# Kernel optimization log

Hardware: AMD Instinct MI355X
Metric: run time of the kernel (lower is better)

Reference implementation:

```python
import jax, jax.numpy as jnp
import numpy as np

N = 50000      # nodes
E = 800000     # edges (avg degree 16)
DIN = 500      # input_dim
HID = 100      # hid_dim (fixed in module)
DOUT = 64      # output_dim
EPS = 1e-5     # LayerNorm eps (torch default)


def _layer_norm(x, g, b):
    mu = jnp.mean(x, axis=-1, keepdims=True)
    var = jnp.var(x, axis=-1, keepdims=True)
    return (x - mu) / jnp.sqrt(var + EPS) * g + b


def _gcn_conv(x, src, tgt, W, b):
    # PyG GCNConv: self-loops + symmetric normalization + linear + scatter-add
    h = x @ W  # [N, out]
    idx = jnp.arange(N)
    src_sl = jnp.concatenate([src, idx])
    tgt_sl = jnp.concatenate([tgt, idx])
    deg = jax.ops.segment_sum(jnp.ones(src_sl.shape, h.dtype), tgt_sl, num_segments=N)
    dinv = jnp.where(deg > 0, deg ** -0.5, 0.0)
    norm = dinv[src_sl] * dinv[tgt_sl]  # [E+N]
    out = jax.ops.segment_sum(h[src_sl] * norm[:, None], tgt_sl, num_segments=N)
    return out + b


def setup_inputs() -> dict:
    key = jax.random.key(0)
    ks = jax.random.split(key, 10)
    glorot = lambda k, fi, fo: jax.random.normal(k, (fi, fo), jnp.float32) * np.float32(1.0 / np.sqrt(fi))
    z = lambda d: jnp.zeros((d,), jnp.float32)
    return dict(
        data_x=jax.random.normal(ks[0], (N, DIN), jnp.float32),
        data_edge_index=jax.random.randint(ks[1], (2, E), 0, N),
        data_edge_attr=jnp.zeros((E,), jnp.int32),  # single relation type
        t_W1=glorot(ks[2], DIN, HID), t_b1=z(HID), t_g1=jnp.ones((HID,), jnp.float32), t_be1=z(HID),
        t_W2=glorot(ks[3], HID, HID), t_b2=z(HID), t_g2=jnp.ones((HID,), jnp.float32), t_be2=z(HID),
        r_Wrel=glorot(ks[4], HID, HID)[None],  # [n_relations=1, H, H]
        r_Wself=glorot(ks[5], HID, HID), r_b=z(HID),
        c1_W=glorot(ks[6], HID, HID), c1_b=z(HID),
        c2_W=glorot(ks[7], HID, DOUT), c2_b=z(DOUT),
    )


def reference(data_x, data_edge_index, data_edge_attr,
              t_W1, t_b1, t_g1, t_be1, t_W2, t_b2, t_g2, t_be2,
              r_Wrel, r_Wself, r_b, c1_W, c1_b, c2_W, c2_b):
    src, tgt = data_edge_index[0], data_edge_index[1]
    # transform: Linear -> LN -> ReLU -> Linear -> LN -> ReLU
    x = jax.nn.relu(_layer_norm(data_x @ t_W1 + t_b1, t_g1, t_be1))
    x = jax.nn.relu(_layer_norm(x @ t_W2 + t_b2, t_g2, t_be2))
    # RGCN, n_relations=1, n_layers=1: per-relation message + self transform
    msgs = x[src] @ r_Wrel[0]  # edge_attr is all relation 0
    x = x @ r_Wself + jax.ops.segment_sum(msgs, tgt, num_segments=N) + r_b
    x = jax.nn.relu(x)  # dropout = identity (eval)
    x = jax.nn.relu(_gcn_conv(x, src, tgt, c1_W, c1_b))
    x = _gcn_conv(x, src, tgt, c2_W, c2_b)
    return jax.nn.log_softmax(x, axis=1)
```

## Files before the change

kernel.cpp:

```cpp
#include <hip/hip_runtime.h>
#include <hip/hip_bf16.h>

typedef __attribute__((ext_vector_type(8))) short short8;
typedef __attribute__((ext_vector_type(8))) unsigned short ushort8;
typedef __attribute__((ext_vector_type(4))) float f32x4;

static constexpr int NN = 50000;
static constexpr int NE = 800000;
static constexpr int SCAN_B = 196;
static constexpr int NBLK = (NN + 63) / 64;

#define MFMA16x16x32 __builtin_amdgcn_mfma_f32_16x16x32_bf16

__device__ __forceinline__ float b2f(unsigned short u){
  unsigned v = ((unsigned)u) << 16;
  return __builtin_bit_cast(float, v);
}
__device__ __forceinline__ unsigned short f2b(float f){
  unsigned x = __builtin_bit_cast(unsigned, f);
  unsigned r = (x + 0x7fffu + ((x >> 16) & 1u)) >> 16;
  return (unsigned short)r;
}
__device__ __forceinline__ short8 u2s(ushort8 v){
  return __builtin_bit_cast(short8, v);
}

__device__ __align__(256) int   g_isf32;
__device__ __align__(256) unsigned short g_W1t  [112 * 512];
__device__ __align__(256) unsigned short g_W2t  [112 * 128];
__device__ __align__(256) unsigned short g_WselfT[112 * 128];
__device__ __align__(256) unsigned short g_WrelT [112 * 128];
__device__ __align__(256) unsigned short g_c1Wt [112 * 128];
__device__ __align__(256) unsigned short g_c2Wt [64 * 128];
__device__ __align__(256) unsigned short g_bufA[(size_t)NN * 128];
__device__ __align__(256) unsigned short g_bufB[(size_t)NN * 128];
__device__ __align__(256) unsigned short g_bufC[(size_t)NN * 128];
__device__ __align__(256) int   g_deg[NN];
__device__ __align__(256) int   g_rowptr[NN + 1];
__device__ __align__(256) int   g_cursor[NN];
__device__ __align__(256) int   g_colidx[NE];
__device__ __align__(256) float g_dinv[NN];
__device__ __align__(256) int   g_partial[256];

__device__ __forceinline__ float ld_in(const void* p, int idx, int isf32){
  if (isf32) return ((const float*)p)[idx];
  return b2f(((const unsigned short*)p)[idx]);
}

__global__ void k_detect_zero(const unsigned short* __restrict__ x){
  if (blockIdx.x == 0){
    __shared__ int sh[256];
    int tid = threadIdx.x;
    int cnt = 0;
    for (int j = 0; j < 16; j++){
      unsigned short h = x[(size_t)(tid * 16 + j) * 2];
      int e = (h >> 7) & 0xFF;
      if (e >= 90 && e <= 160) cnt++;
    }
    sh[tid] = cnt;
    __syncthreads();
    for (int off = 128; off > 0; off >>= 1){
      if (tid < off) sh[tid] += sh[tid + off];
      __syncthreads();
    }
    if (tid == 0) g_isf32 = (sh[0] < 2458) ? 1 : 0;
  } else {
    int i = (blockIdx.x - 1) * 256 + threadIdx.x;
    if (i < NN){ g_deg[i] = 0; g_cursor[i] = 0; }
  }
}

__device__ __forceinline__ void xp_one(const void* W, unsigned short* Wt, int idx,
                                       int K, int Nc, int Kpad, int Npad, int isf32){
  int n = idx / Kpad;
  int k = idx - n * Kpad;
  float v = 0.f;
  if (n < Nc && k < K) v = ld_in(W, k * Nc + n, isf32);
  Wt[(k >> 5) * (Npad * 32) + n * 32 + (k & 31)] = f2b(v);
}
__global__ void k_transpose_all(const void* W1, const void* W2, const void* Wself,
                                const void* Wrel, const void* c1W, const void* c2W){
  int idx = blockIdx.x * 256 + threadIdx.x;
  const int isf32 = g_isf32;
  if (idx < 57344){ xp_one(W1, g_W1t, idx, 500, 100, 512, 112, isf32); return; }
  idx -= 57344;
  if (idx < 14336){ xp_one(W2,    g_W2t,    idx, 100, 100, 128, 112, isf32); return; }
  idx -= 14336;
  if (idx < 14336){ xp_one(Wself, g_WselfT, idx, 100, 100, 128, 112, isf32); return; }
  idx -= 14336;
  if (idx < 14336){ xp_one(Wrel,  g_WrelT,  idx, 100, 100, 128, 112, isf32); return; }
  idx -= 14336;
  if (idx < 14336){ xp_one(c1W,   g_c1Wt,   idx, 100, 100, 128, 112, isf32); return; }
  idx -= 14336;
  if (idx < 8192){  xp_one(c2W,   g_c2Wt,   idx, 100, 64,  128, 64, isf32); }
}

__global__ void k_deg(const int* __restrict__ tgt){
  int e = blockIdx.x * 256 + threadIdx.x;
  if (e < NE) atomicAdd(&g_deg[tgt[e]], 1);
}
__global__ __launch_bounds__(256) void k_scan1(){
  __shared__ int sh[256];
  int t = threadIdx.x;
  int i = blockIdx.x * 256 + t;
  int val = (i < NN) ? g_deg[i] : 0;
  sh[t] = val; __syncthreads();
#pragma unroll
  for (int off = 1; off < 256; off <<= 1){
    int v = (t >= off) ? sh[t - off] : 0;
    __syncthreads(); sh[t] += v; __syncthreads();
  }
  if (i < NN){ g_rowptr[i] = sh[t] - val; g_dinv[i] = rsqrtf((float)(val + 1)); }
  if (t == 255) g_partial[blockIdx.x] = sh[255];
}
__global__ __launch_bounds__(256) void k_scan2(){
  __shared__ int sh[256];
  int t = threadIdx.x;
  int val = (t < SCAN_B) ? g_partial[t] : 0;
  sh[t] = val; __syncthreads();
#pragma unroll
  for (int off = 1; off < 256; off <<= 1){
    int v = (t >= off) ? sh[t - off] : 0;
    __syncthreads(); sh[t] += v; __syncthreads();
  }
  if (t < SCAN_B) g_partial[t] = sh[t] - val;
  if (t == 255) g_rowptr[NN] = sh[255];
}
__global__ __launch_bounds__(256) void k_scan3(){
  int i = blockIdx.x * 256 + threadIdx.x;
  if (i < NN) g_rowptr[i] += g_partial[blockIdx.x];
}
__global__ void k_fill(const int* __restrict__ src, const int* __restrict__ tgt){
  int e = blockIdx.x * 256 + threadIdx.x;
  if (e >= NE) return;
  int t = tgt[e];
  int pos = g_rowptr[t] + atomicAdd(&g_cursor[t], 1);
  g_colidx[pos] = src[e];
}


template<int DO_LN>
__device__ __forceinline__ void wave_epi(const f32x4* acc, unsigned short* dst,
    int rstride, int grow0, int lane, int isf32,
    const void* bias, const void* gm, const void* be){
  const int m = lane & 15;
  const int q = lane >> 4;
  float bf_[7], gf_[7], ef_[7];
#pragma unroll
  for (int t = 0; t < 7; t++){
    int col = t * 16 + m;
    bool ok = col < 100;
    bf_[t] = ok ? ld_in(bias, col, isf32) : 0.f;
    if (DO_LN){
      gf_[t] = ok ? ld_in(gm, col, isf32) : 0.f;
      ef_[t] = ok ? ld_in(be, col, isf32) : 0.f;
    }
  }
#pragma unroll
  for (int r = 0; r < 4; r++){
    int rl = q * 4 + r;
    float vals[7], s1 = 0.f, s2 = 0.f;
#pragma unroll
    for (int t = 0; t < 7; t++){
      int col = t * 16 + m;
      float v = (col < 100) ? (acc[t][r] + bf_[t]) : 0.f;
      vals[t] = v; s1 += v; s2 += v * v;
    }
    if (DO_LN){
#pragma unroll
      for (int msk = 1; msk < 16; msk <<= 1){
        s1 += __shfl_xor(s1, msk, 64);
        s2 += __shfl_xor(s2, msk, 64);
      }
      float mu = s1 * 0.01f;
      float var = fmaxf(s2 * 0.01f - mu * mu, 0.f);
      float rstd = rsqrtf(var + 1e-5f);
#pragma unroll
      for (int t = 0; t < 7; t++)
        vals[t] = (vals[t] - mu) * rstd * gf_[t] + ef_[t];
    }
    if (grow0 + rl < NN){
      unsigned short* orow = dst + (size_t)rl * rstride;
#pragma unroll
      for (int t = 0; t < 7; t++){
        int col = t * 16 + m;
        float y = fmaxf(vals[t], 0.f);
        orow[col] = f2b((col < 100) ? y : 0.f);
      }
      orow[112 + m] = 0;
    }
  }
}

template<int MODE>
__device__ __forceinline__ void agg_tile(const unsigned short* __restrict__ x,
    unsigned short* aggT, int tid, int brow0){
  const int nl = tid >> 2;
  const int c0 = (tid & 3) * 32;
  const int node = min(brow0 + nl, NN - 1);
  const float wt = (MODE != 0) ? g_dinv[node] : 1.f;
  float a[32];
#pragma unroll
  for (int k = 0; k < 32; k++) a[k] = 0.f;
  const int p0 = g_rowptr[node], p1 = g_rowptr[node + 1];
  for (int p = p0; p < p1; p += 4){
    int s[4]; float wj[4];
#pragma unroll
    for (int j = 0; j < 4; j++){
      bool ok = (p + j) < p1;
      s[j] = ok ? g_colidx[p + j] : node;
      wj[j] = ok ? ((MODE != 0) ? g_dinv[s[j]] * wt : 1.f) : 0.f;
    }
    ushort8 r[4][4];
#pragma unroll
    for (int j = 0; j < 4; j++)
#pragma unroll
      for (int u = 0; u < 4; u++)
        r[j][u] = *reinterpret_cast<const ushort8*>(&x[(size_t)s[j] * 128 + c0 + u * 8]);
#pragma unroll
    for (int j = 0; j < 4; j++)
#pragma unroll
      for (int u = 0; u < 4; u++)
#pragma unroll
        for (int k = 0; k < 8; k++)
          a[u * 8 + k] += wj[j] * b2f((unsigned short)r[j][u][k]);
  }
  if (MODE != 0){
    float ws = wt * wt;
#pragma unroll
    for (int u = 0; u < 4; u++){
      ushort8 sv = *reinterpret_cast<const ushort8*>(&x[(size_t)node * 128 + c0 + u * 8]);
#pragma unroll
      for (int k = 0; k < 8; k++) a[u * 8 + k] += ws * b2f((unsigned short)sv[k]);
    }
  }
  unsigned short* arow = aggT + nl * 136 + c0;
#pragma unroll
  for (int u = 0; u < 4; u++){
    ushort8 o;
#pragma unroll
    for (int k = 0; k < 8; k++) o[k] = f2b(a[u * 8 + k]);
    *reinterpret_cast<ushort8*>(&arow[u * 8]) = o;
  }
}


__global__ __launch_bounds__(256, 3) void k_gemm12(const void* __restrict__ Aext,
    const void* b1, const void* gm1, const void* be1,
    const void* b2, const void* gm2, const void* be2){
  __shared__ unsigned short xT[4][16][136];
  const int tid = threadIdx.x;
  const int w = tid >> 6, lane = tid & 63;
  const int m = lane & 15, q = lane >> 4;
  const int row0 = blockIdx.x * 64 + w * 16;
  const int isf32 = g_isf32;
  const int arow = min(row0 + m, NN - 1);

  f32x4 acc[7] = {};
  if (isf32){
    const float* base = (const float*)Aext + (size_t)arow * 500;
#pragma unroll
    for (int h = 0; h < 2; h++){
      f32x4 Ab[16];
#pragma unroll
      for (int kc = 0; kc < 8; kc++){
        int col = (h * 8 + kc) * 32 + q * 8;
        Ab[2 * kc]     = *reinterpret_cast<const f32x4*>(base + min(col, 496));
        Ab[2 * kc + 1] = *reinterpret_cast<const f32x4*>(base + min(col + 4, 496));
      }
      __builtin_amdgcn_sched_barrier(0);
#pragma unroll
      for (int kc = 0; kc < 8; kc++){
        f32x4 lo = Ab[2 * kc], hi = Ab[2 * kc + 1];
        short8 a = {(short)f2b(lo[0]), (short)f2b(lo[1]), (short)f2b(lo[2]), (short)f2b(lo[3]),
                    (short)f2b(hi[0]), (short)f2b(hi[1]), (short)f2b(hi[2]), (short)f2b(hi[3])};
        const unsigned short* bp = g_W1t + (h * 8 + kc) * 3584 + m * 32 + q * 8;
#pragma unroll
        for (int t = 0; t < 7; t++){
          short8 b = *reinterpret_cast<const short8*>(bp + t * 512);
          acc[t] = MFMA16x16x32(a, b, acc[t], 0, 0, 0);
        }
      }
    }
  } else {
    const unsigned short* base = (const unsigned short*)Aext + (size_t)arow * 500;
    ushort4 Ab[32];
#pragma unroll
    for (int kc = 0; kc < 16; kc++){
      int col = kc * 32 + q * 8;
      Ab[2 * kc]     = *reinterpret_cast<const ushort4*>(base + min(col, 496));
      Ab[2 * kc + 1] = *reinterpret_cast<const ushort4*>(base + min(col + 4, 496));
    }
    __builtin_amdgcn_sched_barrier(0);
#pragma unroll
    for (int kc = 0; kc < 16; kc++){
      ushort4 lo = Ab[2 * kc], hi = Ab[2 * kc + 1];
      short8 a = {(short)lo.x, (short)lo.y, (short)lo.z, (short)lo.w,
                  (short)hi.x, (short)hi.y, (short)hi.z, (short)hi.w};
      const unsigned short* bp = g_W1t + kc * 3584 + m * 32 + q * 8;
#pragma unroll
      for (int t = 0; t < 7; t++){
        short8 b = *reinterpret_cast<const short8*>(bp + t * 512);
        acc[t] = MFMA16x16x32(a, b, acc[t], 0, 0, 0);
      }
    }
  }
  wave_epi<1>(acc, &xT[w][0][0], 136, 0, lane, isf32, b1, gm1, be1);

  f32x4 acc2[7] = {};
#pragma unroll
  for (int kc = 0; kc < 4; kc++){
    int k0 = kc * 32 + q * 8;
    short8 a = u2s(*reinterpret_cast<const ushort8*>(&xT[w][m][k0]));
    const unsigned short* bp = g_W2t + kc * 3584 + m * 32 + q * 8;
#pragma unroll
    for (int t = 0; t < 7; t++){
      short8 b = *reinterpret_cast<const short8*>(bp + t * 512);
      acc2[t] = MFMA16x16x32(a, b, acc2[t], 0, 0, 0);
    }
  }
  wave_epi<1>(acc2, g_bufB + (size_t)row0 * 128, 128, row0, lane, isf32, b2, gm2, be2);
}

__global__ __launch_bounds__(256, 3) void k_rgcn_f(const void* rb){
  __shared__ unsigned short aggT[64 * 136];
  const int tid = threadIdx.x;
  const int brow0 = blockIdx.x * 64;
  agg_tile<0>(g_bufB, aggT, tid, brow0);

  const int w = tid >> 6, lane = tid & 63;
  const int m = lane & 15, q = lane >> 4;
  const int row0 = brow0 + w * 16;
  const int arow = min(row0 + m, NN - 1);
  const int isf32 = g_isf32;
  f32x4 acc[7] = {};
#pragma unroll
  for (int kc = 0; kc < 4; kc++){
    int k0 = kc * 32 + q * 8;
    short8 a1 = u2s(*reinterpret_cast<const ushort8*>(&g_bufB[(size_t)arow * 128 + k0]));
    const unsigned short* bp1 = g_WselfT + kc * 3584 + m * 32 + q * 8;
#pragma unroll
    for (int t = 0; t < 7; t++){
      short8 b = *reinterpret_cast<const short8*>(bp1 + t * 512);
      acc[t] = MFMA16x16x32(a1, b, acc[t], 0, 0, 0);
    }
    short8 a2 = u2s(*reinterpret_cast<const ushort8*>(&aggT[(w * 16 + m) * 136 + k0]));
    const unsigned short* bp2 = g_WrelT + kc * 3584 + m * 32 + q * 8;
#pragma unroll
    for (int t = 0; t < 7; t++){
      short8 b = *reinterpret_cast<const short8*>(bp2 + t * 512);
      acc[t] = MFMA16x16x32(a2, b, acc[t], 0, 0, 0);
    }
  }
  wave_epi<0>(acc, g_bufC + (size_t)row0 * 128, 128, row0, lane, isf32, rb, nullptr, nullptr);
}

__global__ __launch_bounds__(256, 3) void k_conv_f(const void* c1b){
  __shared__ unsigned short aggT[64 * 136];
  const int tid = threadIdx.x;
  const int brow0 = blockIdx.x * 64;
  agg_tile<1>(g_bufC, aggT, tid, brow0);

  const int w = tid >> 6, lane = tid & 63;
  const int m = lane & 15, q = lane >> 4;
  const int row0 = brow0 + w * 16;
  const int isf32 = g_isf32;
  unsigned short* tile = aggT + w * 16 * 136;

  f32x4 acc[7] = {};
#pragma unroll
  for (int kc = 0; kc < 4; kc++){
    int k0 = kc * 32 + q * 8;
    short8 a = u2s(*reinterpret_cast<const ushort8*>(&tile[m * 136 + k0]));
    const unsigned short* bp = g_c1Wt + kc * 3584 + m * 32 + q * 8;
#pragma unroll
    for (int t = 0; t < 7; t++){
      short8 b = *reinterpret_cast<const short8*>(bp + t * 512);
      acc[t] = MFMA16x16x32(a, b, acc[t], 0, 0, 0);
    }
  }
  wave_epi<0>(acc, tile, 136, 0, lane, isf32, c1b, nullptr, nullptr);

  f32x4 acc2[4] = {};
#pragma unroll
  for (int kc = 0; kc < 4; kc++){
    int k0 = kc * 32 + q * 8;
    short8 a = u2s(*reinterpret_cast<const ushort8*>(&tile[m * 136 + k0]));
    const unsigned short* bp = g_c2Wt + kc * 2048 + m * 32 + q * 8;
#pragma unroll
    for (int t = 0; t < 4; t++){
      short8 b = *reinterpret_cast<const short8*>(bp + t * 512);
      acc2[t] = MFMA16x16x32(a, b, acc2[t], 0, 0, 0);
    }
  }
#pragma unroll
  for (int r = 0; r < 4; r++){
    int row = row0 + q * 4 + r;
    if (row < NN){
      unsigned short* orow = g_bufA + (size_t)row * 64;
#pragma unroll
      for (int t = 0; t < 4; t++) orow[t * 16 + m] = f2b(acc2[t][r]);
    }
  }
}

__global__ __launch_bounds__(256) void k_agg_lsm(const void* __restrict__ bias,
                                                 void* __restrict__ outv){
  const int isf32 = g_isf32;
  int node = blockIdx.x * 32 + (threadIdx.x >> 3);
  if (node >= NN) return;
  const int c8 = (threadIdx.x & 7) * 8;
  float wt = g_dinv[node];
  float a[4][8];
#pragma unroll
  for (int j = 0; j < 4; j++)
#pragma unroll
    for (int k = 0; k < 8; k++) a[j][k] = 0.f;
  int p0 = g_rowptr[node], p1 = g_rowptr[node + 1];
  for (int p = p0; p < p1; p += 8){
    int sj[8]; float wj[8];
#pragma unroll
    for (int j = 0; j < 8; j++){
      bool ok = (p + j) < p1;
      sj[j] = ok ? g_colidx[p + j] : node;
      wj[j] = ok ? g_dinv[sj[j]] * wt : 0.f;
    }
    ushort8 r[8];
#pragma unroll
    for (int j = 0; j < 8; j++)
      r[j] = *reinterpret_cast<const ushort8*>(&g_bufA[(size_t)sj[j] * 64 + c8]);
#pragma unroll
    for (int j = 0; j < 8; j++)
#pragma unroll
      for (int k = 0; k < 8; k++) a[j & 3][k] += wj[j] * b2f((unsigned short)r[j][k]);
  }
  float ws = wt * wt;
  ushort8 sv = *reinterpret_cast<const ushort8*>(&g_bufA[(size_t)node * 64 + c8]);
#pragma unroll
  for (int k = 0; k < 8; k++) a[0][k] += ws * b2f((unsigned short)sv[k]);

  float v[8], mx = -1e30f;
#pragma unroll
  for (int k = 0; k < 8; k++){
    v[k] = a[0][k] + a[1][k] + a[2][k] + a[3][k] + ld_in(bias, c8 + k, isf32);
    mx = fmaxf(mx, v[k]);
  }
#pragma unroll
  for (int msk = 1; msk < 8; msk <<= 1) mx = fmaxf(mx, __shfl_xor(mx, msk, 64));
  float se = 0.f;
#pragma unroll
  for (int k = 0; k < 8; k++) se += expf(v[k] - mx);
#pragma unroll
  for (int msk = 1; msk < 8; msk <<= 1) se += __shfl_xor(se, msk, 64);
  float lse = logf(se);
  size_t ro = (size_t)node * 64 + c8;
  if (isf32){
    float* o = (float*)outv + ro;
#pragma unroll
    for (int k = 0; k < 8; k++) o[k] = v[k] - mx - lse;
  } else {
    unsigned short* o = (unsigned short*)outv + ro;
#pragma unroll
    for (int k = 0; k < 8; k++) o[k] = f2b(v[k] - mx - lse);
  }
}

extern "C" void kernel_launch(void* const* d_in, const int* in_sizes, int n_in,
                              void* d_out, int out_size, void* d_ws, size_t ws_size,
                              hipStream_t stream){
  (void)in_sizes; (void)n_in; (void)out_size; (void)d_ws; (void)ws_size;
  const void* data_x = d_in[0];
  const int* ei = (const int*)d_in[1];
  const int* src = ei;
  const int* tgt = ei + NE;
  const void *W1 = d_in[3], *b1 = d_in[4], *gm1 = d_in[5], *be1 = d_in[6];
  const void *W2 = d_in[7], *b2 = d_in[8], *gm2 = d_in[9], *be2 = d_in[10];
  const void *Wrel = d_in[11], *Wself = d_in[12], *rb = d_in[13];
  const void *c1W = d_in[14], *c1b = d_in[15];
  const void *c2W = d_in[16], *c2b = d_in[17];

  k_detect_zero<<<1 + (NN + 255) / 256, 256, 0, stream>>>((const unsigned short*)data_x);
  k_transpose_all<<<(122880 + 255) / 256, 256, 0, stream>>>(W1, W2, Wself, Wrel, c1W, c2W);

  k_deg<<<(NE + 255) / 256, 256, 0, stream>>>(tgt);
  k_scan1<<<SCAN_B, 256, 0, stream>>>();
  k_scan2<<<1, 256, 0, stream>>>();
  k_scan3<<<SCAN_B, 256, 0, stream>>>();
  k_fill<<<(NE + 255) / 256, 256, 0, stream>>>(src, tgt);

  k_gemm12<<<NBLK, 256, 0, stream>>>(data_x, b1, gm1, be1, b2, gm2, be2);
  k_rgcn_f<<<NBLK, 256, 0, stream>>>(rb);
  k_conv_f<<<NBLK, 256, 0, stream>>>(c1b);
  k_agg_lsm<<<(NN + 31) / 32, 256, 0, stream>>>(c2b, d_out);
}
```

Before: 478.3 us.

## Stage W1 tiles into LDS via double-buffered global_load_lds; drop fill cursor atomics

The first GEMM now loads all A fragments into registers first, then streams each 32-row K-slice of the transposed W1 into shared memory with double-buffered direct global-to-LDS loads. Each wave reads its B operands from LDS instead of global memory. This targets redundant global/L2 reads of the weights by all four waves, at the cost of a barrier per K step, extra LDS use and higher register pressure from holding 16 A fragments. Separately, the degree kernel records each edge's atomic slot so the CSR fill needs no second atomic pass and no cursor array; the W1 buffer is padded so the final prefetch stays in bounds.

```diff
diff --git a/kernel.cpp b/kernel.cpp
--- a/kernel.cpp
+++ b/kernel.cpp
@@ -26,7 +26,7 @@
 }
 
 __device__ __align__(256) int   g_isf32;
-__device__ __align__(256) unsigned short g_W1t  [112 * 512];
+__device__ __align__(256) unsigned short g_W1t  [112 * 512 + 512];
 __device__ __align__(256) unsigned short g_W2t  [112 * 128];
 __device__ __align__(256) unsigned short g_WselfT[112 * 128];
 __device__ __align__(256) unsigned short g_WrelT [112 * 128];
@@ -37,8 +37,8 @@
 __device__ __align__(256) unsigned short g_bufC[(size_t)NN * 128];
 __device__ __align__(256) int   g_deg[NN];
 __device__ __align__(256) int   g_rowptr[NN + 1];
-__device__ __align__(256) int   g_cursor[NN];
 __device__ __align__(256) int   g_colidx[NE];
+__device__ __align__(256) int   g_epos[NE];
 __device__ __align__(256) float g_dinv[NN];
 __device__ __align__(256) int   g_partial[256];
 
@@ -66,7 +66,7 @@
     if (tid == 0) g_isf32 = (sh[0] < 2458) ? 1 : 0;
   } else {
     int i = (blockIdx.x - 1) * 256 + threadIdx.x;
-    if (i < NN){ g_deg[i] = 0; g_cursor[i] = 0; }
+    if (i < NN) g_deg[i] = 0;
   }
 }
 
@@ -97,7 +97,7 @@
 
 __global__ void k_deg(const int* __restrict__ tgt){
   int e = blockIdx.x * 256 + threadIdx.x;
-  if (e < NE) atomicAdd(&g_deg[tgt[e]], 1);
+  if (e < NE) g_epos[e] = atomicAdd(&g_deg[tgt[e]], 1);
 }
 __global__ __launch_bounds__(256) void k_scan1(){
   __shared__ int sh[256];
@@ -133,9 +133,7 @@
 __global__ void k_fill(const int* __restrict__ src, const int* __restrict__ tgt){
   int e = blockIdx.x * 256 + threadIdx.x;
   if (e >= NE) return;
-  int t = tgt[e];
-  int pos = g_rowptr[t] + atomicAdd(&g_cursor[t], 1);
-  g_colidx[pos] = src[e];
+  g_colidx[g_rowptr[tgt[e]] + g_epos[e]] = src[e];
 }
 
 
@@ -249,6 +247,7 @@
     const void* b1, const void* gm1, const void* be1,
     const void* b2, const void* gm2, const void* be2){
   __shared__ unsigned short xT[4][16][136];
+  __shared__ unsigned short Wst[2][4096];
   const int tid = threadIdx.x;
   const int w = tid >> 6, lane = tid & 63;
   const int m = lane & 15, q = lane >> 4;
@@ -256,7 +255,7 @@
   const int isf32 = g_isf32;
   const int arow = min(row0 + m, NN - 1);
 
-  f32x4 acc[7] = {};
+  short8 afrag[16];
   if (isf32){
     const float* base = (const float*)Aext + (size_t)arow * 500;
 #pragma unroll
@@ -268,43 +267,70 @@
         Ab[2 * kc]     = *reinterpret_cast<const f32x4*>(base + min(col, 496));
         Ab[2 * kc + 1] = *reinterpret_cast<const f32x4*>(base + min(col + 4, 496));
       }
-      __builtin_amdgcn_sched_barrier(0);
 #pragma unroll
       for (int kc = 0; kc < 8; kc++){
         f32x4 lo = Ab[2 * kc], hi = Ab[2 * kc + 1];
-        short8 a = {(short)f2b(lo[0]), (short)f2b(lo[1]), (short)f2b(lo[2]), (short)f2b(lo[3]),
-                    (short)f2b(hi[0]), (short)f2b(hi[1]), (short)f2b(hi[2]), (short)f2b(hi[3])};
-        const unsigned short* bp = g_W1t + (h * 8 + kc) * 3584 + m * 32 + q * 8;
-#pragma unroll
-        for (int t = 0; t < 7; t++){
-          short8 b = *reinterpret_cast<const short8*>(bp + t * 512);
-          acc[t] = MFMA16x16x32(a, b, acc[t], 0, 0, 0);
-        }
+        afrag[h * 8 + kc] = short8{
+          (short)f2b(lo[0]), (short)f2b(lo[1]), (short)f2b(lo[2]), (short)f2b(lo[3]),
+          (short)f2b(hi[0]), (short)f2b(hi[1]), (short)f2b(hi[2]), (short)f2b(hi[3])};
       }
     }
   } else {
     const unsigned short* base = (const unsigned short*)Aext + (size_t)arow * 500;
-    ushort4 Ab[32];
-#pragma unroll
-    for (int kc = 0; kc < 16; kc++){
-      int col = kc * 32 + q * 8;
-      Ab[2 * kc]     = *reinterpret_cast<const ushort4*>(base + min(col, 496));
-      Ab[2 * kc + 1] = *reinterpret_cast<const ushort4*>(base + min(col + 4, 496));
-    }
-    __builtin_amdgcn_sched_barrier(0);
-#pragma unroll
-    for (int kc = 0; kc < 16; kc++){
-      ushort4 lo = Ab[2 * kc], hi = Ab[2 * kc + 1];
-      short8 a = {(short)lo.x, (short)lo.y, (short)lo.z, (short)lo.w,
-                  (short)hi.x, (short)hi.y, (short)hi.z, (short)hi.w};
-      const unsigned short* bp = g_W1t + kc * 3584 + m * 32 + q * 8;
-#pragma unroll
-      for (int t = 0; t < 7; t++){
-        short8 b = *reinterpret_cast<const short8*>(bp + t * 512);
-        acc[t] = MFMA16x16x32(a, b, acc[t], 0, 0, 0);
-      }
-    }
-  }
+#pragma unroll
+    for (int h = 0; h < 2; h++){
+      ushort4 Ab[16];
+#pragma unroll
+      for (int kc = 0; kc < 8; kc++){
+        int col = (h * 8 + kc) * 32 + q * 8;
+        Ab[2 * kc]     = *reinterpret_cast<const ushort4*>(base + min(col, 496));
+        Ab[2 * kc + 1] = *reinterpret_cast<const ushort4*>(base + min(col + 4, 496));
+      }
+#pragma unroll
+      for (int kc = 0; kc < 8; kc++){
+        ushort4 lo = Ab[2 * kc], hi = Ab[2 * kc + 1];
+        afrag[h * 8 + kc] = short8{
+          (short)lo.x, (short)lo.y, (short)lo.z, (short)lo.w,
+          (short)hi.x, (short)hi.y, (short)hi.z, (short)hi.w};
+      }
+    }
+  }
+
+  {
+    const unsigned short* srcp = g_W1t;
+#pragma unroll
+    for (int j = 0; j < 2; j++){
+      int soff = (w * 2 + j) * 512;
+      __builtin_amdgcn_global_load_lds(
+        (const __attribute__((address_space(1))) void*)(srcp + soff + lane * 8),
+        (__attribute__((address_space(3))) void*)(&Wst[0][soff]), 16, 0, 0);
+    }
+  }
+  __syncthreads();
+
+  f32x4 acc[7] = {};
+#pragma unroll
+  for (int kc = 0; kc < 16; kc++){
+    const int cur = kc & 1;
+    if (kc < 15){
+      const unsigned short* srcp = g_W1t + (kc + 1) * 3584;
+#pragma unroll
+      for (int j = 0; j < 2; j++){
+        int soff = (w * 2 + j) * 512;
+        __builtin_amdgcn_global_load_lds(
+          (const __attribute__((address_space(1))) void*)(srcp + soff + lane * 8),
+          (__attribute__((address_space(3))) void*)(&Wst[cur ^ 1][soff]), 16, 0, 0);
+      }
+    }
+    const unsigned short* bp = &Wst[cur][m * 32 + q * 8];
+#pragma unroll
+    for (int t = 0; t < 7; t++){
+      short8 b = *reinterpret_cast<const short8*>(bp + t * 512);
+      acc[t] = MFMA16x16x32(afrag[kc], b, acc[t], 0, 0, 0);
+    }
+    __syncthreads();
+  }
+
   wave_epi<1>(acc, &xT[w][0][0], 136, 0, lane, isf32, b1, gm1, be1);
 
   f32x4 acc2[7] = {};
```

Result: faster. 438.6 us, median of 2 (-8.3%).
